# Performance work log

Hardware: AMD Instinct MI355X
Metric: run time of the kernel (lower is better)

Reference implementation:

```python
import jax, jax.numpy as jnp
import numpy as np
from jax import lax

SEQ, B, IN, H = 2048, 256, 64, 128

def setup_inputs() -> dict:
    key = jax.random.key(0)
    ks = jax.random.split(key, 7)
    seq = jax.random.normal(ks[0], (SEQ, B, IN), dtype=jnp.float32)
    # layer 0: lin_in [H, IN], lin_hidden [H, H] (torch Linear weight layout)
    W_in0 = jax.random.normal(ks[1], (H, IN), dtype=jnp.float32) / np.sqrt(IN)
    W_h0 = jax.random.normal(ks[2], (H, H), dtype=jnp.float32) / np.sqrt(H)
    # layer 1: lin_in [H, H], lin_hidden [H, H]
    W_in1 = jax.random.normal(ks[3], (H, H), dtype=jnp.float32) / np.sqrt(H)
    W_h1 = jax.random.normal(ks[4], (H, H), dtype=jnp.float32) / np.sqrt(H)
    # learned init states, shape [1, H] each (nn.Parameter(torch.zeros(1, H)))
    h0_0 = jnp.zeros((1, H), dtype=jnp.float32)
    h0_1 = jnp.zeros((1, H), dtype=jnp.float32)
    return {"sequence": seq, "W_in0": W_in0, "W_h0": W_h0,
            "W_in1": W_in1, "W_h1": W_h1, "h0_0": h0_0, "h0_1": h0_1}

def _run_layer(x_seq, W_in, W_h, h0):
    # x_seq: [T, B, D_in]; precompute input projection once (same math as per-step)
    xin = jnp.einsum('tbi,hi->tbh', x_seq, W_in)  # [T, B, H]
    h_init = jnp.broadcast_to(h0, (x_seq.shape[1], W_h.shape[0]))
    def step(h, xt):
        h_new = jax.nn.gelu(h @ W_h.T + xt, approximate=False)
        return h_new, h_new
    h_last, ys = lax.scan(step, h_init, xin)
    return ys, h_last

def reference(sequence, W_in0, W_h0, W_in1, W_h1, h0_0, h0_1):
    y0, h0_last = _run_layer(sequence, W_in0, W_h0, h0_0)
    y1, h1_last = _run_layer(y0, W_in1, W_h1, h0_1)
    final_hiddens = jnp.stack([h0_last, h1_last])  # [num_layers, B, H]
    return y1, final_hiddens
```

## Files before the change

kernel.cpp:

```cpp
#include <hip/hip_runtime.h>
#include <math.h>

#define SEQT 2048
#define BATCH 256
#define INDIM 64
#define HDIM 128

typedef float v2f __attribute__((ext_vector_type(2)));
typedef _Float16 f16x2 __attribute__((ext_vector_type(2)));

__device__ __forceinline__ float gelu_fast(float x) {
    const float ax = __builtin_fabsf(x);
    const float z  = ax * 0.70710678118654752f;
    const float t  = __builtin_amdgcn_rcpf(__builtin_fmaf(0.3275911f, z, 1.0f));
    float p = __builtin_fmaf(1.061405429f, t, -1.453152027f);
    p = __builtin_fmaf(p, t, 1.421413741f);
    p = __builtin_fmaf(p, t, -0.284496736f);
    p = __builtin_fmaf(p, t, 0.254829592f);
    p = p * t;
    const float e = __builtin_amdgcn_exp2f(z * z * -1.44269504088896f);
    const float erfv = __builtin_fmaf(-p, e, 1.0f);
    return __builtin_fmaf(0.5f * ax, erfv, 0.5f * x);
}

__device__ __forceinline__ float fdot2(f16x2 a, f16x2 b, float c) {
#if __has_builtin(__builtin_amdgcn_fdot2)
    return __builtin_amdgcn_fdot2(a, b, c, false);
#else
    asm("v_dot2_f32_f16 %0, %1, %2, %0" : "+v"(c) : "v"(a), "v"(b));
    return c;
#endif
}

__device__ __forceinline__ f16x2 bc16(unsigned u) { return __builtin_bit_cast(f16x2, u); }
__device__ __forceinline__ f16x2 cvt_pk(float x, float y) {
    return __builtin_bit_cast(f16x2, __builtin_amdgcn_cvt_pkrtz(x, y));
}
__device__ __forceinline__ unsigned cvt_pk_u(float x, float y) {
    return __builtin_bit_cast(unsigned, __builtin_amdgcn_cvt_pkrtz(x, y));
}

__device__ __forceinline__ void bar_lds() {
    asm volatile("s_waitcnt lgkmcnt(0)\n\ts_barrier" ::: "memory");
}

__global__ __launch_bounds__(256)
void rnn_scan_kernel(
    const float* __restrict__ seq,
    const float* __restrict__ Win0, const float* __restrict__ Wh0,
    const float* __restrict__ Win1, const float* __restrict__ Wh1,
    const float* __restrict__ h00, const float* __restrict__ h01,
    float* __restrict__ out)
{
    const int b = blockIdx.x;
    const int tid = threadIdx.x;
    const int wv = tid >> 6;
    const int l = tid & 63;

    __shared__ __align__(16) unsigned h0f16[4][64];
    __shared__ __align__(16) v2f p1ring[4][64];
    __shared__ __align__(16) v2f x0ring[4][64];
    __shared__ __align__(16) float xring[4][INDIM];

    f16x2 wa[64], wb[64];
    if (wv == 0 || wv == 1) {
        const float* W = (wv == 0) ? Wh0 : Wh1;
        const float* ra = &W[(2 * l) * HDIM];
        const float* rb = &W[(2 * l + 1) * HDIM];
        #pragma unroll
        for (int i = 0; i < 32; ++i) {
            float4 a = reinterpret_cast<const float4*>(ra)[i];
            float4 q = reinterpret_cast<const float4*>(rb)[i];
            wa[2 * i]     = cvt_pk(a.x, a.y);
            wa[2 * i + 1] = cvt_pk(a.z, a.w);
            wb[2 * i]     = cvt_pk(q.x, q.y);
            wb[2 * i + 1] = cvt_pk(q.z, q.w);
        }
    } else if (wv == 2) {
        const float* ra = &Win1[(2 * l) * HDIM];
        const float* rb = &Win1[(2 * l + 1) * HDIM];
        #pragma unroll
        for (int i = 0; i < 32; ++i) {
            float4 a = reinterpret_cast<const float4*>(ra)[i];
            float4 q = reinterpret_cast<const float4*>(rb)[i];
            wa[2 * i]     = cvt_pk(a.x, a.y);
            wa[2 * i + 1] = cvt_pk(a.z, a.w);
            wb[2 * i]     = cvt_pk(q.x, q.y);
            wb[2 * i + 1] = cvt_pk(q.z, q.w);
        }
    } else {
        const float* ra = &Win0[(2 * l) * INDIM];
        const float* rb = &Win0[(2 * l + 1) * INDIM];
        #pragma unroll
        for (int i = 0; i < 16; ++i) {
            float4 a = reinterpret_cast<const float4*>(ra)[i];
            float4 q = reinterpret_cast<const float4*>(rb)[i];
            wa[2 * i]     = cvt_pk(a.x, a.y);
            wa[2 * i + 1] = cvt_pk(a.z, a.w);
            wb[2 * i]     = cvt_pk(q.x, q.y);
            wb[2 * i + 1] = cvt_pk(q.z, q.w);
        }
        #pragma unroll
        for (int i = 32; i < 64; ++i) { wa[i] = (f16x2){0, 0}; wb[i] = (f16x2){0, 0}; }
    }

    unsigned hp_u = 0;
    v2f hf = {0.f, 0.f};
    float xA = 0.f, xB = 0.f, xC = 0.f;
    if (wv == 0) {
        hf = *reinterpret_cast<const v2f*>(&h00[2 * l]);
        hp_u = cvt_pk_u(hf.x, hf.y);
    } else if (wv == 1) {
        hf = *reinterpret_cast<const v2f*>(&h01[2 * l]);
        hp_u = cvt_pk_u(hf.x, hf.y);
    } else if (wv == 3) {
        const size_t base = (size_t)b * INDIM + l;
        xring[0][l] = seq[base];
        xring[1][l] = seq[(size_t)1 * BATCH * INDIM + base];
        xA          = seq[(size_t)2 * BATCH * INDIM + base];
        xB          = seq[(size_t)3 * BATCH * INDIM + base];
        xC          = seq[(size_t)4 * BATCH * INDIM + base];
    }
    __syncthreads();

    const size_t YSZ = (size_t)SEQT * BATCH * HDIM;

    for (int t = 0; t <= SEQT + 3; ++t) {
        if (wv == 0 || wv == 1) {
            const int s = (wv == 0) ? (t - 2) : (t - 4);
            if (s >= 0 && s <= SEQT - 1) {
                v2f xin = (wv == 0) ? x0ring[s & 3][l] : p1ring[s & 3][l];
                float a0 = 0.f, a1 = 0.f, b0 = 0.f, b1 = 0.f;
                #pragma unroll
                for (int j = 0; j < 64; j += 2) {
                    unsigned s0 = __builtin_amdgcn_readlane(hp_u, j);
                    unsigned s1 = __builtin_amdgcn_readlane(hp_u, j + 1);
                    f16x2 p0 = bc16(s0), p1 = bc16(s1);
                    a0 = fdot2(wa[j],     p0, a0);
                    b0 = fdot2(wb[j],     p0, b0);
                    a1 = fdot2(wa[j + 1], p1, a1);
                    b1 = fdot2(wb[j + 1], p1, b1);
                }
                hf.x = gelu_fast((a0 + a1) + xin.x);
                hf.y = gelu_fast((b0 + b1) + xin.y);
                hp_u = cvt_pk_u(hf.x, hf.y);
                if (wv == 0) {
                    h0f16[s & 3][l] = hp_u;
                    if (s == SEQT - 1)
                        *reinterpret_cast<v2f*>(&out[YSZ + (size_t)b * HDIM + 2 * l]) = hf;
                } else {
                    *reinterpret_cast<v2f*>(&out[((size_t)s * BATCH + b) * HDIM + 2 * l]) = hf;
                    if (s == SEQT - 1)
                        *reinterpret_cast<v2f*>(
                            &out[YSZ + (size_t)BATCH * HDIM + (size_t)b * HDIM + 2 * l]) = hf;
                }
            }
        } else if (wv == 2) {
            const int u = t - 3;
            if (u >= 0 && u <= SEQT - 1) {
                const unsigned* hsrc = h0f16[u & 3];
                uint4 q[16];
                #pragma unroll
                for (int i = 0; i < 16; ++i)
                    q[i] = reinterpret_cast<const uint4*>(hsrc)[i];
                float a0 = 0.f, a1 = 0.f, b0 = 0.f, b1 = 0.f;
                #pragma unroll
                for (int i = 0; i < 16; ++i) {
                    const int j = 4 * i;
                    f16x2 p0 = bc16(q[i].x), p1 = bc16(q[i].y);
                    f16x2 p2 = bc16(q[i].z), p3 = bc16(q[i].w);
                    a0 = fdot2(wa[j],     p0, a0);  b0 = fdot2(wb[j],     p0, b0);
                    a1 = fdot2(wa[j + 1], p1, a1);  b1 = fdot2(wb[j + 1], p1, b1);
                    a0 = fdot2(wa[j + 2], p2, a0);  b0 = fdot2(wb[j + 2], p2, b0);
                    a1 = fdot2(wa[j + 3], p3, a1);  b1 = fdot2(wb[j + 3], p3, b1);
                }
                p1ring[u & 3][l] = (v2f){a0 + a1, b0 + b1};
            }
        } else {
            if (t <= SEQT - 1) {
                const float* xs = xring[t & 3];
                float4 xq[16];
                #pragma unroll
                for (int i = 0; i < 16; ++i)
                    xq[i] = reinterpret_cast<const float4*>(xs)[i];
                float a0 = 0.f, a1 = 0.f, b0 = 0.f, b1 = 0.f;
                #pragma unroll
                for (int i = 0; i < 16; ++i) {
                    f16x2 p0 = cvt_pk(xq[i].x, xq[i].y);
                    f16x2 p1 = cvt_pk(xq[i].z, xq[i].w);
                    a0 = fdot2(wa[2 * i],     p0, a0);  b0 = fdot2(wb[2 * i],     p0, b0);
                    a1 = fdot2(wa[2 * i + 1], p1, a1);  b1 = fdot2(wb[2 * i + 1], p1, b1);
                }
                x0ring[t & 3][l] = (v2f){a0 + a1, b0 + b1};
                if (t + 2 <= SEQT - 1) {
                    xring[(t + 2) & 3][l] = xA;
                    xA = xB; xB = xC;
                    int tn = t + 5; if (tn > SEQT - 1) tn = SEQT - 1;
                    xC = seq[(size_t)tn * BATCH * INDIM + (size_t)b * INDIM + l];
                }
            }
        }
        bar_lds();
    }
}

extern "C" void kernel_launch(void* const* d_in, const int* in_sizes, int n_in,
                              void* d_out, int out_size, void* d_ws, size_t ws_size,
                              hipStream_t stream) {
    const float* seq  = (const float*)d_in[0];
    const float* Win0 = (const float*)d_in[1];
    const float* Wh0  = (const float*)d_in[2];
    const float* Win1 = (const float*)d_in[3];
    const float* Wh1  = (const float*)d_in[4];
    const float* h00  = (const float*)d_in[5];
    const float* h01  = (const float*)d_in[6];

    rnn_scan_kernel<<<dim3(BATCH), dim3(256), 0, stream>>>(
        seq, Win0, Wh0, Win1, Wh1, h00, h01, (float*)d_out);
}
```

Baseline: 1.516 ms.

## Process two batch rows per block with 512-thread blocks

```diff
diff --git a/kernel.cpp b/kernel.cpp
--- a/kernel.cpp
+++ b/kernel.cpp
@@ -44,7 +44,7 @@
     asm volatile("s_waitcnt lgkmcnt(0)\n\ts_barrier" ::: "memory");
 }
 
-__global__ __launch_bounds__(256)
+__global__ __launch_bounds__(512)
 void rnn_scan_kernel(
     const float* __restrict__ seq,
     const float* __restrict__ Win0, const float* __restrict__ Wh0,
@@ -52,21 +52,22 @@
     const float* __restrict__ h00, const float* __restrict__ h01,
     float* __restrict__ out)
 {
-    const int b = blockIdx.x;
     const int tid = threadIdx.x;
     const int wv = tid >> 6;
     const int l = tid & 63;
-
-    __shared__ __align__(16) unsigned h0f16[4][64];
-    __shared__ __align__(16) v2f p1ring[4][64];
-    __shared__ __align__(16) v2f x0ring[4][64];
-    __shared__ __align__(16) float xring[4][INDIM];
+    const int role = wv >> 1;
+    const int row  = wv & 1;
+    const int b = blockIdx.x * 2 + row;
+
+    __shared__ __align__(16) unsigned h0f16[2][4][64];
+    __shared__ __align__(16) v2f p1ring[2][4][64];
+    __shared__ __align__(16) v2f x0ring[2][4][64];
+    __shared__ __align__(16) float xring[2][4][INDIM];
 
     f16x2 wa[64], wb[64];
-    if (wv == 0 || wv == 1) {
-        const float* W = (wv == 0) ? Wh0 : Wh1;
-        const float* ra = &W[(2 * l) * HDIM];
-        const float* rb = &W[(2 * l + 1) * HDIM];
+    if (role == 0) {
+        const float* ra = &Wh0[(2 * l) * HDIM];
+        const float* rb = &Wh0[(2 * l + 1) * HDIM];
         #pragma unroll
         for (int i = 0; i < 32; ++i) {
             float4 a = reinterpret_cast<const float4*>(ra)[i];
@@ -76,7 +77,19 @@
             wb[2 * i]     = cvt_pk(q.x, q.y);
             wb[2 * i + 1] = cvt_pk(q.z, q.w);
         }
-    } else if (wv == 2) {
+    } else if (role == 1) {
+        const float* ra = &Wh1[(2 * l) * HDIM];
+        const float* rb = &Wh1[(2 * l + 1) * HDIM];
+        #pragma unroll
+        for (int i = 0; i < 32; ++i) {
+            float4 a = reinterpret_cast<const float4*>(ra)[i];
+            float4 q = reinterpret_cast<const float4*>(rb)[i];
+            wa[2 * i]     = cvt_pk(a.x, a.y);
+            wa[2 * i + 1] = cvt_pk(a.z, a.w);
+            wb[2 * i]     = cvt_pk(q.x, q.y);
+            wb[2 * i + 1] = cvt_pk(q.z, q.w);
+        }
+    } else if (role == 2) {
         const float* ra = &Win1[(2 * l) * HDIM];
         const float* rb = &Win1[(2 * l + 1) * HDIM];
         #pragma unroll
@@ -107,29 +120,29 @@
     unsigned hp_u = 0;
     v2f hf = {0.f, 0.f};
     float xA = 0.f, xB = 0.f, xC = 0.f;
-    if (wv == 0) {
+    if (role == 0) {
         hf = *reinterpret_cast<const v2f*>(&h00[2 * l]);
         hp_u = cvt_pk_u(hf.x, hf.y);
-    } else if (wv == 1) {
+    } else if (role == 1) {
         hf = *reinterpret_cast<const v2f*>(&h01[2 * l]);
         hp_u = cvt_pk_u(hf.x, hf.y);
-    } else if (wv == 3) {
+    } else if (role == 3) {
         const size_t base = (size_t)b * INDIM + l;
-        xring[0][l] = seq[base];
-        xring[1][l] = seq[(size_t)1 * BATCH * INDIM + base];
-        xA          = seq[(size_t)2 * BATCH * INDIM + base];
-        xB          = seq[(size_t)3 * BATCH * INDIM + base];
-        xC          = seq[(size_t)4 * BATCH * INDIM + base];
+        xring[row][0][l] = seq[base];
+        xring[row][1][l] = seq[(size_t)1 * BATCH * INDIM + base];
+        xA               = seq[(size_t)2 * BATCH * INDIM + base];
+        xB               = seq[(size_t)3 * BATCH * INDIM + base];
+        xC               = seq[(size_t)4 * BATCH * INDIM + base];
     }
     __syncthreads();
 
     const size_t YSZ = (size_t)SEQT * BATCH * HDIM;
 
     for (int t = 0; t <= SEQT + 3; ++t) {
-        if (wv == 0 || wv == 1) {
-            const int s = (wv == 0) ? (t - 2) : (t - 4);
+        if (role == 0 || role == 1) {
+            const int s = (role == 0) ? (t - 2) : (t - 4);
             if (s >= 0 && s <= SEQT - 1) {
-                v2f xin = (wv == 0) ? x0ring[s & 3][l] : p1ring[s & 3][l];
+                v2f xin = (role == 0) ? x0ring[row][s & 3][l] : p1ring[row][s & 3][l];
                 float a0 = 0.f, a1 = 0.f, b0 = 0.f, b1 = 0.f;
                 #pragma unroll
                 for (int j = 0; j < 64; j += 2) {
@@ -144,8 +157,8 @@
                 hf.x = gelu_fast((a0 + a1) + xin.x);
                 hf.y = gelu_fast((b0 + b1) + xin.y);
                 hp_u = cvt_pk_u(hf.x, hf.y);
-                if (wv == 0) {
-                    h0f16[s & 3][l] = hp_u;
+                if (role == 0) {
+                    h0f16[row][s & 3][l] = hp_u;
                     if (s == SEQT - 1)
                         *reinterpret_cast<v2f*>(&out[YSZ + (size_t)b * HDIM + 2 * l]) = hf;
                 } else {
@@ -155,10 +168,10 @@
                             &out[YSZ + (size_t)BATCH * HDIM + (size_t)b * HDIM + 2 * l]) = hf;
                 }
             }
-        } else if (wv == 2) {
+        } else if (role == 2) {
             const int u = t - 3;
             if (u >= 0 && u <= SEQT - 1) {
-                const unsigned* hsrc = h0f16[u & 3];
+                const unsigned* hsrc = h0f16[row][u & 3];
                 uint4 q[16];
                 #pragma unroll
                 for (int i = 0; i < 16; ++i)
@@ -174,11 +187,11 @@
                     a0 = fdot2(wa[j + 2], p2, a0);  b0 = fdot2(wb[j + 2], p2, b0);
                     a1 = fdot2(wa[j + 3], p3, a1);  b1 = fdot2(wb[j + 3], p3, b1);
                 }
-                p1ring[u & 3][l] = (v2f){a0 + a1, b0 + b1};
+                p1ring[row][u & 3][l] = (v2f){a0 + a1, b0 + b1};
             }
         } else {
             if (t <= SEQT - 1) {
-                const float* xs = xring[t & 3];
+                const float* xs = xring[row][t & 3];
                 float4 xq[16];
                 #pragma unroll
                 for (int i = 0; i < 16; ++i)
@@ -191,9 +204,9 @@
                     a0 = fdot2(wa[2 * i],     p0, a0);  b0 = fdot2(wb[2 * i],     p0, b0);
                     a1 = fdot2(wa[2 * i + 1], p1, a1);  b1 = fdot2(wb[2 * i + 1], p1, b1);
                 }
-                x0ring[t & 3][l] = (v2f){a0 + a1, b0 + b1};
+                x0ring[row][t & 3][l] = (v2f){a0 + a1, b0 + b1};
                 if (t + 2 <= SEQT - 1) {
-                    xring[(t + 2) & 3][l] = xA;
+                    xring[row][(t + 2) & 3][l] = xA;
                     xA = xB; xB = xC;
                     int tn = t + 5; if (tn > SEQT - 1) tn = SEQT - 1;
                     xC = seq[(size_t)tn * BATCH * INDIM + (size_t)b * INDIM + l];
@@ -215,6 +228,6 @@
     const float* h00  = (const float*)d_in[5];
     const float* h01  = (const float*)d_in[6];
 
-    rnn_scan_kernel<<<dim3(BATCH), dim3(256), 0, stream>>>(
+    rnn_scan_kernel<<<dim3(BATCH / 2), dim3(512), 0, stream>>>(
         seq, Win0, Wh0, Win1, Wh1, h00, h01, (float*)d_out);
 }
```

After: 2.293 ms. 1.51x slower.
